# Performance work log

Hardware: AMD Instinct MI355X
Metric: run time of the kernel (lower is better)

The kernel has to match this reference:

```python
import jax, jax.numpy as jnp
import numpy as np
from jax import lax

EPS = 2.220446049250313e-16  # np.finfo(float).eps, as in the torch source
DN3 = ('NCDHW', 'OIDHW', 'NCDHW')
DN2 = ('NCHW', 'OIHW', 'NCHW')


def setup_inputs() -> dict:
    key = jax.random.key(0)
    k1, k2, k3 = jax.random.split(key, 3)
    x = jax.random.normal(k1, (256, 256), dtype=jnp.float32)
    filts_temp = jax.random.normal(k2, (8, 1, 2, 9, 9), dtype=jnp.float32)    # [Ft,1,T=2,kh,kw]
    filts_notemp = jax.random.normal(k3, (8, 1, 1, 9, 9), dtype=jnp.float32)  # [Fn,1,1,kh,kw]
    return {"x": x, "filts_temp": filts_temp, "filts_notemp": filts_notemp, "num_rfs": 2}


def _forward(x, filts_temp, filts_notemp, num_rfs):
    kh, kw = filts_temp.shape[3], filts_temp.shape[4]
    corr_x = num_rfs * kh  # torch uses shape[3]
    corr_y = num_rfs * kw  # torch uses shape[4]
    num_filts = filts_temp.shape[0] + filts_notemp.shape[0]

    # x -> [1,1,2,H,W]: duplicate the frame along a temporal axis of length 2
    xv = jnp.broadcast_to(x, (2,) + x.shape)[None, None]

    # fixed-filter temporal conv3d + ReLU (halved)
    x_temp = jax.nn.relu(
        lax.conv_general_dilated(xv, filts_temp, (1, 1, 1), 'VALID', dimension_numbers=DN3) / 2
    )  # [1,Ft,1,H',W']
    # non-temporal conv on the last time slice
    x_notemp = jax.nn.relu(
        lax.conv_general_dilated(xv[:, :, -1:, :, :], filts_notemp, (1, 1, 1), 'VALID',
                                 dimension_numbers=DN3)
    )  # [1,Fn,1,H',W']

    xc = jnp.concatenate([x_temp, x_notemp], axis=1)  # [1,nf,1,H',W']
    # normalize across the filter channel (divisive normalization)
    x1 = xc / (jnp.sum(xc, axis=1, keepdims=True) + EPS)

    H_, W_ = x1.shape[3], x1.shape[4]
    x1f = x1[0, :, 0]  # [nf,H',W']
    # central crop used as correlation templates
    templates = x1f[:, corr_y:H_ - corr_y, corr_x:W_ - corr_x]  # [nf, H'-2cy, W'-2cx]

    # windowed pairwise cross-channel correlation: the torch conv3d with depth-kernel 1
    # is exactly a batched 2D valid cross-correlation (batch = depth index j,
    # out-channel = template index i)
    out = lax.conv_general_dilated(x1f[:, None], templates[:, None], (1, 1), 'VALID',
                                   dimension_numbers=DN2)  # [j, i, 2cy+1, 2cx+1]
    x2 = jnp.transpose(out, (1, 0, 2, 3))[None]  # [1, i, j, 2cy+1, 2cx+1]
    # note: source divides by (y_max-2*corr_y)*(x_max-2*corr_y) (corr_y twice) -- kept faithful
    x2 = x2 / ((H_ - 2 * corr_y) * (W_ - 2 * corr_y))

    x1_out = x1f[None, None]  # [1,1,nf,H',W']
    return (x1_out, x2)


def reference(x, filts_temp, filts_notemp, num_rfs):
    return _forward(x, filts_temp, filts_notemp, num_rfs)
```

## Files before the change

### kernel.cpp

```cpp
#include <hip/hip_runtime.h>
#include <hip/hip_fp8.h>
#include <cstdint>

typedef unsigned short u16;
typedef unsigned int   u32;
typedef unsigned long long u64;
typedef float  f32x16 __attribute__((ext_vector_type(16)));
typedef float  f32x4  __attribute__((ext_vector_type(4)));
typedef u32    u32x2  __attribute__((ext_vector_type(2)));
typedef u32    u32x4  __attribute__((ext_vector_type(4)));

#define OUT1 984064
#define OUT2 350464

#define XD_STRIDE  1015808
#define TMPL_OFFB  8126464
#define PART_OFFB  8900608
#define PART_ELEMS (6*OUT2)
#define XC_OFFB    17311744

__global__ __launch_bounds__(256) void k1_conv(
    const float* __restrict__ x, const float* __restrict__ ft,
    const float* __restrict__ fnt, float* __restrict__ out1,
    u16* __restrict__ Xc) {
  __shared__ float xt[24][25];
  __shared__ float wsm[1296];
  const int tid = threadIdx.x;
  const int lx = tid & 15, ly = tid >> 4;
  const int bx = blockIdx.x, by = blockIdx.y;
  for (int idx = tid; idx < 1296; idx += 256) {
    int c = idx / 81, s = idx - (idx / 81) * 81;
    wsm[idx] = (c < 8) ? 0.5f * (ft[c*162 + s] + ft[c*162 + 81 + s])
                       : fnt[(c-8)*81 + s];
  }
  for (int idx = tid; idx < 576; idx += 256) {
    int ry = idx / 24, rx = idx - ry * 24;
    int gy = by*16 + ry; gy = gy > 255 ? 255 : gy;
    int gx = bx*16 + rx; gx = gx > 255 ? 255 : gx;
    xt[ry][rx] = x[gy*256 + gx];
  }
  __syncthreads();
  const int xg = bx*16 + lx, yg = by*16 + ly;
  if (yg >= 248) return;
  float s[16];
#pragma unroll
  for (int c = 0; c < 16; ++c) s[c] = 0.f;
  const bool valid = (xg < 248);
  if (valid) {
#pragma unroll
    for (int u = 0; u < 9; ++u)
#pragma unroll
      for (int v = 0; v < 9; ++v) {
        float xv = xt[ly + u][lx + v];
#pragma unroll
        for (int c = 0; c < 16; ++c)
          s[c] = __builtin_fmaf(xv, wsm[c*81 + u*9 + v], s[c]);
      }
    float sum = 2.2204460492503131e-16f;
#pragma unroll
    for (int c = 0; c < 16; ++c) { s[c] = s[c] > 0.f ? s[c] : 0.f; sum += s[c]; }
    float inv = 1.f / sum;
#pragma unroll
    for (int c = 0; c < 16; ++c) s[c] *= inv;
  }
#pragma unroll
  for (int c = 0; c < 16; ++c) {
    u16 hb = 0;
    if (valid) {
      out1[c*61504 + yg*248 + xg] = s[c];
      u32 ub = __builtin_bit_cast(u32, s[c]);
      hb = (u16)((ub + 0x7fffu + ((ub >> 16) & 1u)) >> 16);
    }
    if (xg < 264) Xc[(c*248 + yg)*264 + xg] = hb;
  }
}

__device__ __forceinline__ u32 pk4_fp8(u32 b0, u32 b1) {
  float f0 = __builtin_bit_cast(float, b0 << 16);
  float f1 = __builtin_bit_cast(float, b0 & 0xFFFF0000u);
  float f2 = __builtin_bit_cast(float, b1 << 16);
  float f3 = __builtin_bit_cast(float, b1 & 0xFFFF0000u);
  __hip_fp8_e4m3 e0(f0), e1(f1), e2(f2), e3(f3);
  return (u32)e0.__x | ((u32)e1.__x << 8) | ((u32)e2.__x << 16) | ((u32)e3.__x << 24);
}

__global__ __launch_bounds__(256) void k1b_expand(
    const u16* __restrict__ Xc, unsigned char* __restrict__ ws8,
    float* __restrict__ partial) {
  const int cid = blockIdx.x*256 + threadIdx.x;
  for (int z = cid; z < PART_ELEMS; z += gridDim.x*256) partial[z] = 0.f;
  const u32* src = (const u32*)Xc;
  if (cid < 507904) {
    int np = cid & 7;
    int r1 = cid >> 3;
    int row = r1 % 248;
    int r2  = r1 / 248;
    int vb  = r2 & 31;
    int d   = r2 >> 5;
    int colb = (d & ~1) + 8*vb;
    u32 wout[4];
#pragma unroll
    for (int h = 0; h < 2; ++h) {
      int n = 2*np + h;
      int so = (n*248 + row)*132 + (colb >> 1);
      u32 a0 = src[so], a1 = src[so+1], a2 = src[so+2], a3 = src[so+3], a4 = src[so+4];
      u32 b0, b1, b2, b3;
      if (d & 1) {
        b0 = (a0 >> 16) | (a1 << 16); b1 = (a1 >> 16) | (a2 << 16);
        b2 = (a2 >> 16) | (a3 << 16); b3 = (a3 >> 16) | (a4 << 16);
      } else { b0 = a0; b1 = a1; b2 = a2; b3 = a3; }
      wout[h*2]     = pk4_fp8(b0, b1);
      wout[h*2 + 1] = pk4_fp8(b2, b3);
    }
    u32x4 v = { wout[0], wout[1], wout[2], wout[3] };
    *(u32x4*)(ws8 + ((size_t)((d*32 + vb)*248 + row))*128 + np*16) = v;
  } else if (cid < 507904 + 48384) {
    int t  = cid - 507904;
    int np = t & 7;
    int r1 = t >> 3;
    int tr = r1 % 216;
    int vb = r1 / 216;
    u32x4 v = {0u, 0u, 0u, 0u};
    if (tr < 212 && vb < 27) {
#pragma unroll
      for (int h = 0; h < 2; ++h) {
        int n = 2*np + h;
        int so = (n*248 + tr + 18)*132 + ((18 + 8*vb) >> 1);
        u32 b0 = src[so], b1 = src[so+1], b2 = src[so+2], b3 = src[so+3];
        if (vb == 26) { b2 = 0u; b3 = 0u; }
        v[h*2]     = pk4_fp8(b0, b1);
        v[h*2 + 1] = pk4_fp8(b2, b3);
      }
    }
    *(u32x4*)(ws8 + TMPL_OFFB + ((size_t)(vb*216 + tr))*128 + np*16) = v;
  }
}

#define F_LD(k,m,c) fl[(k)*1024 + (((m)&3) + 4*((m)>>3))*64 + ((c) + 32*(((m)>>2)&1))]

#define LOADA(q,SO) asm volatile("buffer_load_dwordx2 %0, %1, %2, %3 offen" \
  : "=v"(A[q]) : "v"(voffA[q]), "s"(srdA), "s"(SO));
#define LOADB(t,SO) asm volatile("buffer_load_dwordx2 %0, %1, %2, %3 offen" \
  : "=v"(B[t]) : "v"(voffB[t]), "s"(srdB), "s"(SO));
#define WT(N,X,Y) asm volatile("s_waitcnt vmcnt(" #N ")" : "+v"(X), "+v"(Y) ::);
#define MF5(t) { long _bb = __builtin_bit_cast(long, B[t]); \
  acc[0]=__builtin_amdgcn_mfma_f32_32x32x16_fp8_fp8(__builtin_bit_cast(long,A[t+0]),_bb,acc[0],0,0,0); \
  acc[1]=__builtin_amdgcn_mfma_f32_32x32x16_fp8_fp8(__builtin_bit_cast(long,A[t+1]),_bb,acc[1],0,0,0); \
  acc[2]=__builtin_amdgcn_mfma_f32_32x32x16_fp8_fp8(__builtin_bit_cast(long,A[t+2]),_bb,acc[2],0,0,0); \
  acc[3]=__builtin_amdgcn_mfma_f32_32x32x16_fp8_fp8(__builtin_bit_cast(long,A[t+3]),_bb,acc[3],0,0,0); \
  acc[4]=__builtin_amdgcn_mfma_f32_32x32x16_fp8_fp8(__builtin_bit_cast(long,A[t+4]),_bb,acc[4],0,0,0); }

__global__ __launch_bounds__(256, 2) void k2_corr(
    const unsigned char* __restrict__ Ximg3, const unsigned char* __restrict__ Tmpl3,
    float* __restrict__ partial) {
  __shared__ float fl[5120];
  const int bid = blockIdx.x;
  const int d   = bid & 7;
  const int m0  = bid >> 3;
  const int jq  = m0 % 5;
  const int cmb = m0 / 5;
  const int g   = cmb & 3;
  const int uq  = cmb >> 2;
  const int j   = d + 8*jq;
  if (j >= 37) return;
  const int U0  = 72*uq;
  const int R0  = 10*g + U0;
  const int tid  = threadIdx.x;
  const int lane = tid & 63;
  const int w    = tid >> 6;
  const int fn16 = lane & 15;
  const int fuu  = (lane >> 4) & 1;
  const int fg   = lane >> 5;

  u64 pa = (u64)(Ximg3 + d*XD_STRIDE + jq*31744);
  u64 pb = (u64)(Tmpl3);
  u32x4 srdA = { (u32)pa, (u32)(pa >> 32), 0xFFFFFFFFu, 0x00020000u };
  u32x4 srdB = { (u32)pb, (u32)(pb >> 32), 0xFFFFFFFFu, 0x00020000u };
  int voffA[13], voffB[9];
#pragma unroll
  for (int q = 0; q < 13; ++q) {
    int r = R0 + fuu + 18*w + 2*q;
    if (r > 247) r = 247;
    voffA[q] = fg*31744 + fn16*8 + r*128;
  }
#pragma unroll
  for (int t = 0; t < 9; ++t)
    voffB[t] = fg*27648 + fn16*8 + (U0 + fuu + 18*w + 2*t)*128;

  f32x16 acc[5];
#pragma unroll
  for (int k = 0; k < 5; ++k)
#pragma unroll
    for (int q = 0; q < 16; ++q) acc[k][q] = 0.f;

  u32x2 A[13], B[9];
  { int sa = 0, sb = 0;
    LOADA(0,sa) LOADB(0,sb) LOADA(1,sa) LOADB(1,sb)
    LOADA(2,sa) LOADB(2,sb) LOADA(3,sa) LOADB(3,sb)
    LOADA(4,sa) LOADB(4,sb) LOADA(5,sa) LOADB(5,sb)
    LOADA(6,sa) LOADB(6,sb) LOADA(7,sa) LOADB(7,sb)
    LOADA(8,sa) LOADA(9,sa) LOADA(10,sa) LOADA(11,sa) LOADA(12,sa) LOADB(8,sb) }

#pragma unroll 1
  for (int sv = 0; sv < 13; ++sv) {
    const int sa = (sv + 1)*63488, sb = (sv + 1)*55296;
    WT(13, A[4],  B[0])  MF5(0) LOADA(0,sa) LOADB(0,sb)
    WT(13, A[5],  B[1])  MF5(1) LOADA(1,sa) LOADB(1,sb)
    WT(13, A[6],  B[2])  MF5(2) LOADA(2,sa) LOADB(2,sb)
    WT(13, A[7],  B[3])  MF5(3) LOADA(3,sa) LOADB(3,sb)
    WT(13, A[8],  B[4])  MF5(4) LOADA(4,sa) LOADB(4,sb)
    WT(14, A[9],  B[5])  MF5(5) LOADA(5,sa) LOADB(5,sb)
    WT(15, A[10], B[6])  MF5(6) LOADA(6,sa) LOADB(6,sb)
    WT(16, A[11], B[7])  MF5(7) LOADA(7,sa) LOADB(7,sb)
    WT(16, A[12], B[8])  MF5(8)
    LOADA(8,sa) LOADA(9,sa) LOADA(10,sa) LOADA(11,sa) LOADA(12,sa) LOADB(8,sb)
  }
  WT(13, A[4],  B[0])  MF5(0)
  WT(11, A[5],  B[1])  MF5(1)
  WT(9,  A[6],  B[2])  MF5(2)
  WT(7,  A[7],  B[3])  MF5(3)
  WT(5,  A[8],  B[4])  MF5(4)
  WT(4,  A[9],  B[5])  MF5(5)
  WT(3,  A[10], B[6])  MF5(6)
  WT(2,  A[11], B[7])  MF5(7)
  WT(0,  A[12], B[8])  MF5(8)
  __syncthreads();

  for (int z = tid; z < 5120; z += 256) fl[z] = 0.f;
  __syncthreads();
  for (int ww = 0; ww < 4; ++ww) {
    if (w == ww) {
#pragma unroll
      for (int k = 0; k < 5; ++k) {
        if (!(g == 3 && k == 4)) {
#pragma unroll
          for (int q = 0; q < 16; ++q)
            fl[k*1024 + q*64 + lane] += acc[k][q];
        }
      }
    }
    __syncthreads();
  }

  const int n = (tid >> 4) & 15;
  const int o = tid & 15;
  float* slab = partial + (uq*2 + (g & 1)) * OUT2;
  for (int ii = 0; ii < 11; ++ii) {
    const int i = 10*g - 1 + ii;
    if (i < 0 || i >= 37) continue;
    const int dd = ii - 1;
    float v;
    if (!(dd & 1)) {
      const int k = dd >> 1;
      v = F_LD(k, n, o) + F_LD(k, n+16, o+16);
    } else {
      v = 0.f;
      if (dd >= 1) v += F_LD((dd-1) >> 1, n+16, o);
      const int kr = (dd+1) >> 1;
      if (kr <= 4) v += F_LD(kr, n, o+16);
    }
    slab[(o*16 + n)*1369 + i*37 + j] = v;
  }
}

__global__ __launch_bounds__(256) void k3_reduce(
    const float* __restrict__ partial, float* __restrict__ out2) {
  const int idx = blockIdx.x*256 + threadIdx.x;
  if (idx >= OUT2/4) return;
  f32x4 s = {0.f, 0.f, 0.f, 0.f};
#pragma unroll
  for (int t = 0; t < 6; ++t) {
    f32x4 v = *(const f32x4*)(partial + t*OUT2 + idx*4);
    s[0] += v[0]; s[1] += v[1]; s[2] += v[2]; s[3] += v[3];
  }
  const float sc = 1.0f / 44944.0f;
  s[0] *= sc; s[1] *= sc; s[2] *= sc; s[3] *= sc;
  *(f32x4*)(out2 + idx*4) = s;
}

extern "C" void kernel_launch(void* const* d_in, const int* in_sizes, int n_in,
                              void* d_out, int out_size, void* d_ws, size_t ws_size,
                              hipStream_t stream) {
  (void)in_sizes; (void)n_in; (void)out_size; (void)ws_size;
  const float* x   = (const float*)d_in[0];
  const float* ft  = (const float*)d_in[1];
  const float* fnt = (const float*)d_in[2];
  float* out = (float*)d_out;
  char*  ws  = (char*)d_ws;
  unsigned char* Ximg3 = (unsigned char*)ws;
  unsigned char* Tmpl3 = (unsigned char*)(ws + TMPL_OFFB);
  float* partial = (float*)(ws + PART_OFFB);
  u16*   Xc      = (u16*)(ws + XC_OFFB);

  k1_conv<<<dim3(17, 16), 256, 0, stream>>>(x, ft, fnt, out, Xc);
  k1b_expand<<<2173, 256, 0, stream>>>(Xc, (unsigned char*)ws, partial);
  k2_corr<<<480, 256, 0, stream>>>(Ximg3, Tmpl3, partial);
  k3_reduce<<<343, 256, 0, stream>>>(partial, out + OUT1);
}
```

Before: 68.48 us.

## Split correlation over stencil-row chunks per block, waves over row groups

Reassigns work in the correlation kernel. Each wave now owns a row-offset group, and each block handles a subset of the outer sv iterations instead of all of them. Each iteration streams a long 36-step A/B buffer-load pipeline through rotating 12-entry register rings. Results are accumulated into twelve partial slabs with read-modify-write, and the final reduce sums all twelve. The aim is shorter per-block serial chains and better load/MFMA overlap, at the cost of doubled partial-buffer traffic and a dependence on the partial buffer being zeroed.

```diff
diff --git a/kernel.cpp b/kernel.cpp
--- a/kernel.cpp
+++ b/kernel.cpp
@@ -16,8 +16,8 @@
 #define XD_STRIDE  1015808
 #define TMPL_OFFB  8126464
 #define PART_OFFB  8900608
-#define PART_ELEMS (6*OUT2)
-#define XC_OFFB    17311744
+#define PART_ELEMS (12*OUT2)
+#define XC_OFFB    25722880
 
 __global__ __launch_bounds__(256) void k1_conv(
     const float* __restrict__ x, const float* __restrict__ ft,
@@ -138,17 +138,23 @@
 
 #define F_LD(k,m,c) fl[(k)*1024 + (((m)&3) + 4*((m)>>3))*64 + ((c) + 32*(((m)>>2)&1))]
 
-#define LOADA(q,SO) asm volatile("buffer_load_dwordx2 %0, %1, %2, %3 offen" \
-  : "=v"(A[q]) : "v"(voffA[q]), "s"(srdA), "s"(SO));
-#define LOADB(t,SO) asm volatile("buffer_load_dwordx2 %0, %1, %2, %3 offen" \
-  : "=v"(B[t]) : "v"(voffB[t]), "s"(srdB), "s"(SO));
-#define WT(N,X,Y) asm volatile("s_waitcnt vmcnt(" #N ")" : "+v"(X), "+v"(Y) ::);
-#define MF5(t) { long _bb = __builtin_bit_cast(long, B[t]); \
-  acc[0]=__builtin_amdgcn_mfma_f32_32x32x16_fp8_fp8(__builtin_bit_cast(long,A[t+0]),_bb,acc[0],0,0,0); \
-  acc[1]=__builtin_amdgcn_mfma_f32_32x32x16_fp8_fp8(__builtin_bit_cast(long,A[t+1]),_bb,acc[1],0,0,0); \
-  acc[2]=__builtin_amdgcn_mfma_f32_32x32x16_fp8_fp8(__builtin_bit_cast(long,A[t+2]),_bb,acc[2],0,0,0); \
-  acc[3]=__builtin_amdgcn_mfma_f32_32x32x16_fp8_fp8(__builtin_bit_cast(long,A[t+3]),_bb,acc[3],0,0,0); \
-  acc[4]=__builtin_amdgcn_mfma_f32_32x32x16_fp8_fp8(__builtin_bit_cast(long,A[t+4]),_bb,acc[4],0,0,0); }
+#define LDA(P) asm volatile("buffer_load_dwordx2 %0, %1, %2, %3 offen" \
+  : "=v"(Ar[(P)%12]) : "v"(voffA0), "s"(srdA), "s"(sa + (P)*256));
+#define LDAT(P) asm volatile("buffer_load_dwordx2 %0, %1, %2, %3 offen" \
+  : "=v"(Ar[(P)%12]) : "v"(voffAt[(P)-36]), "s"(srdA), "s"(sa));
+#define LDB(T) asm volatile("buffer_load_dwordx2 %0, %1, %2, %3 offen" \
+  : "=v"(Br[(T)%12]) : "v"(voffB0), "s"(srdB), "s"(sb + (T)*256));
+#define WTT(N,t) asm volatile("s_waitcnt vmcnt(" #N ")" \
+  : "+v"(Ar[((t)+4)%12]), "+v"(Br[(t)%12]) ::);
+#define MF5T(t) { long _bb = __builtin_bit_cast(long, Br[(t)%12]); \
+  acc[0]=__builtin_amdgcn_mfma_f32_32x32x16_fp8_fp8(__builtin_bit_cast(long,Ar[((t)+0)%12]),_bb,acc[0],0,0,0); \
+  acc[1]=__builtin_amdgcn_mfma_f32_32x32x16_fp8_fp8(__builtin_bit_cast(long,Ar[((t)+1)%12]),_bb,acc[1],0,0,0); \
+  acc[2]=__builtin_amdgcn_mfma_f32_32x32x16_fp8_fp8(__builtin_bit_cast(long,Ar[((t)+2)%12]),_bb,acc[2],0,0,0); \
+  acc[3]=__builtin_amdgcn_mfma_f32_32x32x16_fp8_fp8(__builtin_bit_cast(long,Ar[((t)+3)%12]),_bb,acc[3],0,0,0); \
+  acc[4]=__builtin_amdgcn_mfma_f32_32x32x16_fp8_fp8(__builtin_bit_cast(long,Ar[((t)+4)%12]),_bb,acc[4],0,0,0); }
+#define TSF(t,N) WTT(N,t) MF5T(t) LDA((t)+11) LDB((t)+11)
+#define TSA(t,N) WTT(N,t) MF5T(t) LDAT((t)+11)
+#define TSN(t,N) WTT(N,t) MF5T(t)
 
 __global__ __launch_bounds__(256, 2) void k2_corr(
     const unsigned char* __restrict__ Ximg3, const unsigned char* __restrict__ Tmpl3,
@@ -158,34 +164,35 @@
   const int d   = bid & 7;
   const int m0  = bid >> 3;
   const int jq  = m0 % 5;
-  const int cmb = m0 / 5;
-  const int g   = cmb & 3;
-  const int uq  = cmb >> 2;
+  const int r   = m0 / 5;
+  const int uq  = r % 3;
+  const int svq = r / 3;
   const int j   = d + 8*jq;
   if (j >= 37) return;
-  const int U0  = 72*uq;
-  const int R0  = 10*g + U0;
   const int tid  = threadIdx.x;
   const int lane = tid & 63;
   const int w    = tid >> 6;
   const int fn16 = lane & 15;
   const int fuu  = (lane >> 4) & 1;
   const int fg   = lane >> 5;
+  const int U0   = 72*uq;
+  const int R0   = 10*w + U0;
+  const int sv0  = (svq < 2) ? 4*svq : 8 + 3*(svq - 2);
+  const int nsv  = (svq < 2) ? 4 : 3;
 
   u64 pa = (u64)(Ximg3 + d*XD_STRIDE + jq*31744);
   u64 pb = (u64)(Tmpl3);
   u32x4 srdA = { (u32)pa, (u32)(pa >> 32), 0xFFFFFFFFu, 0x00020000u };
   u32x4 srdB = { (u32)pb, (u32)(pb >> 32), 0xFFFFFFFFu, 0x00020000u };
-  int voffA[13], voffB[9];
-#pragma unroll
-  for (int q = 0; q < 13; ++q) {
-    int r = R0 + fuu + 18*w + 2*q;
-    if (r > 247) r = 247;
-    voffA[q] = fg*31744 + fn16*8 + r*128;
-  }
-#pragma unroll
-  for (int t = 0; t < 9; ++t)
-    voffB[t] = fg*27648 + fn16*8 + (U0 + fuu + 18*w + 2*t)*128;
+  const int voffA0 = fg*31744 + fn16*8 + (R0 + fuu)*128;
+  const int voffB0 = fg*27648 + fn16*8 + (U0 + fuu)*128;
+  int voffAt[4];
+#pragma unroll
+  for (int i = 0; i < 4; ++i) {
+    int row = R0 + fuu + 2*(36 + i);
+    if (row > 247) row = 247;
+    voffAt[i] = fg*31744 + fn16*8 + row*128;
+  }
 
   f32x16 acc[5];
 #pragma unroll
@@ -193,46 +200,34 @@
 #pragma unroll
     for (int q = 0; q < 16; ++q) acc[k][q] = 0.f;
 
-  u32x2 A[13], B[9];
-  { int sa = 0, sb = 0;
-    LOADA(0,sa) LOADB(0,sb) LOADA(1,sa) LOADB(1,sb)
-    LOADA(2,sa) LOADB(2,sb) LOADA(3,sa) LOADB(3,sb)
-    LOADA(4,sa) LOADB(4,sb) LOADA(5,sa) LOADB(5,sb)
-    LOADA(6,sa) LOADB(6,sb) LOADA(7,sa) LOADB(7,sb)
-    LOADA(8,sa) LOADA(9,sa) LOADA(10,sa) LOADA(11,sa) LOADA(12,sa) LOADB(8,sb) }
-
+  u32x2 Ar[12], Br[12];
 #pragma unroll 1
-  for (int sv = 0; sv < 13; ++sv) {
-    const int sa = (sv + 1)*63488, sb = (sv + 1)*55296;
-    WT(13, A[4],  B[0])  MF5(0) LOADA(0,sa) LOADB(0,sb)
-    WT(13, A[5],  B[1])  MF5(1) LOADA(1,sa) LOADB(1,sb)
-    WT(13, A[6],  B[2])  MF5(2) LOADA(2,sa) LOADB(2,sb)
-    WT(13, A[7],  B[3])  MF5(3) LOADA(3,sa) LOADB(3,sb)
-    WT(13, A[8],  B[4])  MF5(4) LOADA(4,sa) LOADB(4,sb)
-    WT(14, A[9],  B[5])  MF5(5) LOADA(5,sa) LOADB(5,sb)
-    WT(15, A[10], B[6])  MF5(6) LOADA(6,sa) LOADB(6,sb)
-    WT(16, A[11], B[7])  MF5(7) LOADA(7,sa) LOADB(7,sb)
-    WT(16, A[12], B[8])  MF5(8)
-    LOADA(8,sa) LOADA(9,sa) LOADA(10,sa) LOADA(11,sa) LOADA(12,sa) LOADB(8,sb)
-  }
-  WT(13, A[4],  B[0])  MF5(0)
-  WT(11, A[5],  B[1])  MF5(1)
-  WT(9,  A[6],  B[2])  MF5(2)
-  WT(7,  A[7],  B[3])  MF5(3)
-  WT(5,  A[8],  B[4])  MF5(4)
-  WT(4,  A[9],  B[5])  MF5(5)
-  WT(3,  A[10], B[6])  MF5(6)
-  WT(2,  A[11], B[7])  MF5(7)
-  WT(0,  A[12], B[8])  MF5(8)
+  for (int sv = sv0; sv < sv0 + nsv; ++sv) {
+    const int sa = sv*63488, sb = sv*55296;
+    LDA(0) LDB(0) LDA(1) LDB(1) LDA(2) LDB(2) LDA(3) LDB(3) LDA(4) LDB(4)
+    LDA(5) LDB(5) LDA(6) LDB(6) LDA(7) LDB(7) LDA(8) LDB(8) LDA(9) LDB(9)
+    LDA(10) LDB(10)
+    TSF(0,13)  TSF(1,13)  TSF(2,13)  TSF(3,13)  TSF(4,13)
+    TSF(5,13)  TSF(6,13)  TSF(7,13)  TSF(8,13)  TSF(9,13)
+    TSF(10,13) TSF(11,13) TSF(12,13) TSF(13,13) TSF(14,13)
+    TSF(15,13) TSF(16,13) TSF(17,13) TSF(18,13) TSF(19,13)
+    TSF(20,13) TSF(21,13) TSF(22,13) TSF(23,13) TSF(24,13)
+    TSA(25,13) TSA(26,12) TSA(27,11) TSA(28,10)
+    TSN(29,9)  TSN(30,7)  TSN(31,5)  TSN(32,3)  TSN(33,2)
+    TSN(34,1)  TSN(35,0)
+  }
   __syncthreads();
 
-  for (int z = tid; z < 5120; z += 256) fl[z] = 0.f;
-  __syncthreads();
-  for (int ww = 0; ww < 4; ++ww) {
-    if (w == ww) {
+  const int n = (tid >> 4) & 15;
+  const int o = tid & 15;
+  float* slab = partial + (svq*3 + uq) * OUT2;
+  for (int g2 = 0; g2 < 4; ++g2) {
+    for (int z = tid; z < 5120; z += 256) fl[z] = 0.f;
+    __syncthreads();
+    if (w == g2) {
 #pragma unroll
       for (int k = 0; k < 5; ++k) {
-        if (!(g == 3 && k == 4)) {
+        if (!(g2 == 3 && k == 4)) {
 #pragma unroll
           for (int q = 0; q < 16; ++q)
             fl[k*1024 + q*64 + lane] += acc[k][q];
@@ -240,26 +235,23 @@
       }
     }
     __syncthreads();
-  }
-
-  const int n = (tid >> 4) & 15;
-  const int o = tid & 15;
-  float* slab = partial + (uq*2 + (g & 1)) * OUT2;
-  for (int ii = 0; ii < 11; ++ii) {
-    const int i = 10*g - 1 + ii;
-    if (i < 0 || i >= 37) continue;
-    const int dd = ii - 1;
-    float v;
-    if (!(dd & 1)) {
-      const int k = dd >> 1;
-      v = F_LD(k, n, o) + F_LD(k, n+16, o+16);
-    } else {
-      v = 0.f;
-      if (dd >= 1) v += F_LD((dd-1) >> 1, n+16, o);
-      const int kr = (dd+1) >> 1;
-      if (kr <= 4) v += F_LD(kr, n, o+16);
-    }
-    slab[(o*16 + n)*1369 + i*37 + j] = v;
+    for (int ii = 0; ii < 11; ++ii) {
+      const int i = 10*g2 - 1 + ii;
+      if (i < 0 || i >= 37) continue;
+      const int dd = ii - 1;
+      float v;
+      if (!(dd & 1)) {
+        const int k = dd >> 1;
+        v = F_LD(k, n, o) + F_LD(k, n+16, o+16);
+      } else {
+        v = 0.f;
+        if (dd >= 1) v += F_LD((dd-1) >> 1, n+16, o);
+        const int kr = (dd+1) >> 1;
+        if (kr <= 4) v += F_LD(kr, n, o+16);
+      }
+      slab[(o*16 + n)*1369 + i*37 + j] += v;
+    }
+    __syncthreads();
   }
 }
 
@@ -269,7 +261,7 @@
   if (idx >= OUT2/4) return;
   f32x4 s = {0.f, 0.f, 0.f, 0.f};
 #pragma unroll
-  for (int t = 0; t < 6; ++t) {
+  for (int t = 0; t < 12; ++t) {
     f32x4 v = *(const f32x4*)(partial + t*OUT2 + idx*4);
     s[0] += v[0]; s[1] += v[1]; s[2] += v[2]; s[3] += v[3];
   }
```

After: 153.8 us. 2.25x slower.
